# Kernel optimization log

Measured on AMD Instinct MI355X. Metric: run time of the kernel, lower is better.

## Reference

```python
import jax, jax.numpy as jnp
import numpy as np

D_MODEL = 256
NUM_HEADS = 4
EPS = 1e-6


def setup_inputs() -> dict:
    key = jax.random.key(0)
    ks = jax.random.split(key, 9)
    B, T, D = 4, 2048, D_MODEL
    scale = 1.0 / np.sqrt(D)
    inp = {
        "x": jax.random.normal(ks[0], (B, T, D), dtype=jnp.float32),
        "Wq": jax.random.normal(ks[1], (D, D), dtype=jnp.float32) * scale,
        "bq": jnp.zeros((D,), dtype=jnp.float32),
        "Wk": jax.random.normal(ks[2], (D, D), dtype=jnp.float32) * scale,
        "bk": jnp.zeros((D,), dtype=jnp.float32),
        "Wv": jax.random.normal(ks[3], (D, D), dtype=jnp.float32) * scale,
        "bv": jnp.zeros((D,), dtype=jnp.float32),
        "Wo": jax.random.normal(ks[4], (D, D), dtype=jnp.float32) * scale,
        "bo": jnp.zeros((D,), dtype=jnp.float32),
    }
    return inp


def _feature_map(a):
    # F.elu(x) + 1.0
    return jax.nn.elu(a) + 1.0


def reference(x, Wq, bq, Wk, bk, Wv, bv, Wo, bo):
    B, T, D = x.shape
    H = NUM_HEADS
    dh = D // H
    Q = _feature_map((x @ Wq + bq).reshape(B, T, H, dh))
    K = _feature_map((x @ Wk + bk).reshape(B, T, H, dh))
    V = (x @ Wv + bv).reshape(B, T, H, dh)
    # outer-product state: (B,T,H,dh,dh), cumulative over time
    KV = jnp.einsum('bthd,bthm->bthdm', K, V)
    S = jnp.cumsum(KV, axis=1)
    Z = jnp.cumsum(K, axis=1)
    out = jnp.einsum('bthd,bthdm->bthm', Q, S)
    denom = jnp.einsum('bthd,bthd->bth', Q, Z)[..., None] + EPS
    out = (out / denom).reshape(B, T, D)
    return out @ Wo + bo
```

## Files before the change

### kernel.cpp

```cpp
#include <hip/hip_runtime.h>
#include <hip/hip_bf16.h>

#define D_MODEL 256
#define NHEADS 4
#define DHEAD 64
#define BATCH 4
#define TSEQ 2048
#define CHUNK 64
#define NCHUNK (TSEQ / CHUNK)
#define NTOK (BATCH * TSEQ)
#define NBH (BATCH * NHEADS)
#define EPSV 1e-6f
#define LSTRF 68

typedef __bf16 bf16x8 __attribute__((ext_vector_type(8)));
typedef float f32x4 __attribute__((ext_vector_type(4)));
typedef unsigned short us8 __attribute__((ext_vector_type(8)));

__device__ __forceinline__ float elu1(float a) {
    return a > 0.0f ? a + 1.0f : __expf(a);
}

__device__ __forceinline__ unsigned short f2bf(float f) {
    __hip_bfloat16 h = __float2bfloat16(f);
    return __builtin_bit_cast(unsigned short, h);
}

__device__ __forceinline__ float bf2f(unsigned short u) {
    return __bfloat162float(__builtin_bit_cast(__hip_bfloat16, u));
}

__device__ __forceinline__ bf16x8 frag8(const float* p) {
    const float4 x = *reinterpret_cast<const float4*>(p);
    const float4 y = *reinterpret_cast<const float4*>(p + 4);
    us8 u;
    u[0] = f2bf(x.x); u[1] = f2bf(x.y); u[2] = f2bf(x.z); u[3] = f2bf(x.w);
    u[4] = f2bf(y.x); u[5] = f2bf(y.y); u[6] = f2bf(y.z); u[7] = f2bf(y.w);
    return __builtin_bit_cast(bf16x8, u);
}

__device__ __forceinline__ void gld_lds16(const void* g, void* l) {
    __builtin_amdgcn_global_load_lds(
        (const __attribute__((address_space(1))) void*)g,
        (__attribute__((address_space(3))) void*)l, 16, 0, 0);
}

__global__ __launch_bounds__(256) void convert_x_kernel(
    const float* __restrict__ x, unsigned short* __restrict__ xb)
{
    const int i = (blockIdx.x * 256 + threadIdx.x) * 8;
    const float4 a = *reinterpret_cast<const float4*>(&x[i]);
    const float4 b = *reinterpret_cast<const float4*>(&x[i + 4]);
    ushort4 u0 = { f2bf(a.x), f2bf(a.y), f2bf(a.z), f2bf(a.w) };
    ushort4 u1 = { f2bf(b.x), f2bf(b.y), f2bf(b.z), f2bf(b.w) };
    *reinterpret_cast<ushort4*>(&xb[i]) = u0;
    *reinterpret_cast<ushort4*>(&xb[i + 4]) = u1;
}

__global__ __launch_bounds__(256) void convert_w_kernel(
    const float* __restrict__ Wq, const float* __restrict__ Wk,
    const float* __restrict__ Wv, const float* __restrict__ Wo,
    unsigned short* __restrict__ Wt, unsigned short* __restrict__ Wot)
{
    __shared__ float Ls[64][65];
    const int tid = threadIdx.x;
    const int wi = blockIdx.x >> 4;
    const int ti = blockIdx.x & 15;
    const int k0 = (ti >> 2) * 64, n0 = (ti & 3) * 64;
    const float* W = wi == 0 ? Wq : wi == 1 ? Wk : wi == 2 ? Wv : Wo;
#pragma unroll
    for (int i = 0; i < 16; ++i) {
        const int idx = i * 256 + tid;
        const int r = idx >> 6, c = idx & 63;
        Ls[r][c] = W[(size_t)(k0 + r) * D_MODEL + n0 + c];
    }
    __syncthreads();
    unsigned short* outp = (wi < 3) ? (Wt + (size_t)(wi * 256 + n0) * D_MODEL + k0)
                                    : (Wot + (size_t)n0 * D_MODEL + k0);
#pragma unroll
    for (int i = 0; i < 16; ++i) {
        const int idx = i * 256 + tid;
        const int rn = idx >> 6, ck = idx & 63;
        outp[(size_t)rn * D_MODEL + ck] = f2bf(Ls[ck][rn]);
    }
}

template<int MODE>
__global__ __launch_bounds__(256) void mfma_gemm_kernel(
    const unsigned short* __restrict__ A,
    const unsigned short* __restrict__ Bt,
    const float* __restrict__ b0, const float* __restrict__ b1,
    const float* __restrict__ b2,
    void* __restrict__ O0, void* __restrict__ O1, void* __restrict__ O2)
{
    __shared__ __align__(16) unsigned short As[128 * 64];
    __shared__ __align__(16) unsigned short Bs[128 * 64];
    const int tid = threadIdx.x;
    const int wave = tid >> 6, lane = tid & 63;
    const int la = lane & 15, q = lane >> 4;
    const int wm = (wave >> 1) * 64, wn = (wave & 1) * 64;

    int mtile, ntile;
    if (MODE == 0) { ntile = blockIdx.x % 6; mtile = blockIdx.x / 6; }
    else           { ntile = blockIdx.x & 1; mtile = blockIdx.x >> 1; }
    const int m0 = mtile * 128, n0 = ntile * 128;

    const unsigned short* Ab = A  + (size_t)m0 * D_MODEL;
    const unsigned short* Bb = Bt + (size_t)n0 * D_MODEL;

    f32x4 acc[4][4];
#pragma unroll
    for (int i = 0; i < 4; ++i)
#pragma unroll
        for (int j = 0; j < 4; ++j) acc[i][j] = (f32x4){0.f, 0.f, 0.f, 0.f};

    for (int k0 = 0; k0 < D_MODEL; k0 += 64) {
#pragma unroll
        for (int i = 0; i < 4; ++i) {
            const int bslot = i * 256 + wave * 64;
            const int slot = bslot + lane;
            const int m = slot >> 3, s = slot & 7;
            const int g = s ^ (m & 7);
            gld_lds16(Ab + (size_t)m * D_MODEL + k0 + g * 8, &As[bslot * 8]);
            gld_lds16(Bb + (size_t)m * D_MODEL + k0 + g * 8, &Bs[bslot * 8]);
        }
        __syncthreads();

        bf16x8 af[4][2], bfr[4][2];
#pragma unroll
        for (int i = 0; i < 4; ++i) {
#pragma unroll
            for (int kh = 0; kh < 2; ++kh) {
                const int g = kh * 4 + q;
                const int m = wm + i * 16 + la;
                af[i][kh] = *reinterpret_cast<const bf16x8*>(
                    &As[m * 64 + ((g ^ (m & 7)) << 3)]);
                const int n = wn + i * 16 + la;
                bfr[i][kh] = *reinterpret_cast<const bf16x8*>(
                    &Bs[n * 64 + ((g ^ (n & 7)) << 3)]);
            }
        }
#pragma unroll
        for (int mi = 0; mi < 4; ++mi)
#pragma unroll
            for (int ni = 0; ni < 4; ++ni) {
                acc[mi][ni] = __builtin_amdgcn_mfma_f32_16x16x32_bf16(
                    af[mi][0], bfr[ni][0], acc[mi][ni], 0, 0, 0);
                acc[mi][ni] = __builtin_amdgcn_mfma_f32_16x16x32_bf16(
                    af[mi][1], bfr[ni][1], acc[mi][ni], 0, 0, 0);
            }
        __syncthreads();
    }

#pragma unroll
    for (int mi = 0; mi < 4; ++mi) {
#pragma unroll
        for (int ni = 0; ni < 4; ++ni) {
            const int row = m0 + wm + mi * 16 + q * 4;
            const int col = n0 + wn + ni * 16 + la;
            if (MODE == 0) {
                const int which = col >> 8;
                const int cl = col & 255;
                unsigned short* Out = (unsigned short*)
                    (which == 0 ? O0 : which == 1 ? O1 : O2);
                const float* bias = which == 0 ? b0 : which == 1 ? b1 : b2;
                const int act = (which < 2);
                const float bv = bias[cl];
#pragma unroll
                for (int r = 0; r < 4; ++r) {
                    float v = acc[mi][ni][r] + bv;
                    if (act) v = elu1(v);
                    Out[(size_t)(row + r) * D_MODEL + cl] = f2bf(v);
                }
            } else {
                float* Out = (float*)O0;
                const float bv = b0[col];
#pragma unroll
                for (int r = 0; r < 4; ++r)
                    Out[(size_t)(row + r) * D_MODEL + col] = acc[mi][ni][r] + bv;
            }
        }
    }
}

__global__ __launch_bounds__(256) void chunksum_kernel(
    const unsigned short* __restrict__ Kb, const unsigned short* __restrict__ Vb,
    float* __restrict__ Pt, float* __restrict__ Zc)
{
    __shared__ float Ktf[DHEAD * LSTRF];
    __shared__ float Vtf[DHEAD * LSTRF];
    const int tid = threadIdx.x;
    const int c  = blockIdx.x % NCHUNK;
    const int bh = blockIdx.x / NCHUNK;
    const int b = bh / NHEADS, h = bh % NHEADS;
    const size_t gbase = ((size_t)(b * TSEQ + c * CHUNK)) * D_MODEL + h * DHEAD;

#pragma unroll
    for (int i = 0; i < 16; ++i) {
        const int idx = i * 256 + tid;
        const int t = idx >> 6, d = idx & 63;
        Ktf[d * LSTRF + t] = bf2f(Kb[gbase + (size_t)t * D_MODEL + d]);
        Vtf[d * LSTRF + t] = bf2f(Vb[gbase + (size_t)t * D_MODEL + d]);
    }
    __syncthreads();

    const int wave = tid >> 6, lane = tid & 63;
    const int la = lane & 15, q = lane >> 4;
    const int wm = (wave >> 1) * 32, wn = (wave & 1) * 32;

    f32x4 acc[2][2];
#pragma unroll
    for (int i = 0; i < 2; ++i)
#pragma unroll
        for (int j = 0; j < 2; ++j) acc[i][j] = (f32x4){0.f, 0.f, 0.f, 0.f};

#pragma unroll
    for (int ks = 0; ks < 2; ++ks) {
        const int ko = ks * 32 + q * 8;
        const bf16x8 a0  = frag8(&Vtf[(wm + la) * LSTRF + ko]);
        const bf16x8 a1  = frag8(&Vtf[(wm + 16 + la) * LSTRF + ko]);
        const bf16x8 bb0 = frag8(&Ktf[(wn + la) * LSTRF + ko]);
        const bf16x8 bb1 = frag8(&Ktf[(wn + 16 + la) * LSTRF + ko]);
        acc[0][0] = __builtin_amdgcn_mfma_f32_16x16x32_bf16(a0, bb0, acc[0][0], 0, 0, 0);
        acc[0][1] = __builtin_amdgcn_mfma_f32_16x16x32_bf16(a0, bb1, acc[0][1], 0, 0, 0);
        acc[1][0] = __builtin_amdgcn_mfma_f32_16x16x32_bf16(a1, bb0, acc[1][0], 0, 0, 0);
        acc[1][1] = __builtin_amdgcn_mfma_f32_16x16x32_bf16(a1, bb1, acc[1][1], 0, 0, 0);
    }

    float* Pb = Pt + (size_t)blockIdx.x * (DHEAD * DHEAD);
#pragma unroll
    for (int mi = 0; mi < 2; ++mi)
#pragma unroll
        for (int ni = 0; ni < 2; ++ni) {
            const int row = wm + mi * 16 + q * 4;
            const int col = wn + ni * 16 + la;
#pragma unroll
            for (int r = 0; r < 4; ++r)
                Pb[(row + r) * DHEAD + col] = acc[mi][ni][r];
        }

    if (tid < DHEAD) {
        float z = 0.f;
        for (int t = 0; t < CHUNK; ++t) z += Ktf[tid * LSTRF + t];
        Zc[(size_t)blockIdx.x * DHEAD + tid] = z;
    }
}

__global__ __launch_bounds__(256) void prefix_kernel(
    float* __restrict__ P, float* __restrict__ Zc)
{
    const int tid = threadIdx.x;
    if (blockIdx.x < NBH * 16) {
        const int bh = blockIdx.x >> 4;
        const int e = ((blockIdx.x & 15) << 8) + tid;
        const size_t base = (size_t)bh * NCHUNK * (DHEAD * DHEAD) + e;
        float v[NCHUNK];
#pragma unroll
        for (int c = 0; c < NCHUNK; ++c) v[c] = P[base + (size_t)c * (DHEAD * DHEAD)];
        float s = 0.f;
#pragma unroll
        for (int c = 0; c < NCHUNK; ++c) {
            const float t = v[c];
            P[base + (size_t)c * (DHEAD * DHEAD)] = s;
            s += t;
        }
    } else {
        const int j = ((int)(blockIdx.x - NBH * 16) << 8) + tid;
        if (j < NBH * DHEAD) {
            const int bh = j >> 6, d = j & 63;
            float v[NCHUNK];
#pragma unroll
            for (int c = 0; c < NCHUNK; ++c) v[c] = Zc[(bh * NCHUNK + c) * DHEAD + d];
            float s = 0.f;
#pragma unroll
            for (int c = 0; c < NCHUNK; ++c) {
                const float t = v[c];
                Zc[(bh * NCHUNK + c) * DHEAD + d] = s;
                s += t;
            }
        }
    }
}

__global__ __launch_bounds__(256) void chunkout_kernel(
    const unsigned short* __restrict__ Qb, const unsigned short* __restrict__ Kb,
    const unsigned short* __restrict__ Vb,
    const float* __restrict__ Pt, const float* __restrict__ Zx,
    unsigned short* __restrict__ Ob)
{
    __shared__ float Qs[CHUNK * LSTRF];
    __shared__ float Ks[CHUNK * LSTRF];
    __shared__ float Vtf[DHEAD * LSTRF];
    __shared__ float At[CHUNK * LSTRF];
    __shared__ float zsh[DHEAD];
    __shared__ float dnm[CHUNK];

    const int tid = threadIdx.x;
    const int c  = blockIdx.x % NCHUNK;
    const int bh = blockIdx.x / NCHUNK;
    const int b = bh / NHEADS, h = bh % NHEADS;
    const size_t gbase = ((size_t)(b * TSEQ + c * CHUNK)) * D_MODEL + h * DHEAD;
    const float* Pp = Pt + (size_t)blockIdx.x * (DHEAD * DHEAD);

#pragma unroll
    for (int i = 0; i < 16; ++i) {
        const int idx = i * 256 + tid;
        const int t = idx >> 6, d = idx & 63;
        const float qv = bf2f(Qb[gbase + (size_t)t * D_MODEL + d]);
        const float kv = bf2f(Kb[gbase + (size_t)t * D_MODEL + d]);
        const float vv = bf2f(Vb[gbase + (size_t)t * D_MODEL + d]);
        Qs[t * LSTRF + d]  = qv;
        Ks[t * LSTRF + d]  = kv;
        Vtf[d * LSTRF + t] = vv;
    }
    if (tid < DHEAD) zsh[tid] = Zx[((size_t)bh * NCHUNK + c) * DHEAD + tid];
    __syncthreads();

    const int wave = tid >> 6, lane = tid & 63;
    const int la = lane & 15, q = lane >> 4;
    const int wt = (wave >> 1) * 32, wn = (wave & 1) * 32;

    f32x4 acc[2][2];
#pragma unroll
    for (int i = 0; i < 2; ++i)
#pragma unroll
        for (int j = 0; j < 2; ++j) acc[i][j] = (f32x4){0.f, 0.f, 0.f, 0.f};
#pragma unroll
    for (int ks = 0; ks < 2; ++ks) {
        const int ko = ks * 32 + q * 8;
        const bf16x8 a0  = frag8(&Qs[(wt + la) * LSTRF + ko]);
        const bf16x8 a1  = frag8(&Qs[(wt + 16 + la) * LSTRF + ko]);
        const bf16x8 bb0 = frag8(&Ks[(wn + la) * LSTRF + ko]);
        const bf16x8 bb1 = frag8(&Ks[(wn + 16 + la) * LSTRF + ko]);
        acc[0][0] = __builtin_amdgcn_mfma_f32_16x16x32_bf16(a0, bb0, acc[0][0], 0, 0, 0);
        acc[0][1] = __builtin_amdgcn_mfma_f32_16x16x32_bf16(a0, bb1, acc[0][1], 0, 0, 0);
        acc[1][0] = __builtin_amdgcn_mfma_f32_16x16x32_bf16(a1, bb0, acc[1][0], 0, 0, 0);
        acc[1][1] = __builtin_amdgcn_mfma_f32_16x16x32_bf16(a1, bb1, acc[1][1], 0, 0, 0);
    }
#pragma unroll
    for (int mi = 0; mi < 2; ++mi)
#pragma unroll
        for (int ni = 0; ni < 2; ++ni) {
            const int t0 = wt + mi * 16 + q * 4;
            const int s  = wn + ni * 16 + la;
#pragma unroll
            for (int r = 0; r < 4; ++r)
                At[(t0 + r) * LSTRF + s] = (s <= t0 + r) ? acc[mi][ni][r] : 0.f;
        }
    __syncthreads();

    if (tid < CHUNK) {
        float dv = 0.f;
        for (int s = 0; s < CHUNK; ++s) dv += At[tid * LSTRF + s];
        for (int d = 0; d < DHEAD; ++d) dv = fmaf(Qs[tid * LSTRF + d], zsh[d], dv);
        dnm[tid] = dv + EPSV;
    }
    __syncthreads();

    f32x4 o[2][2];
#pragma unroll
    for (int i = 0; i < 2; ++i)
#pragma unroll
        for (int j = 0; j < 2; ++j) o[i][j] = (f32x4){0.f, 0.f, 0.f, 0.f};
#pragma unroll
    for (int ks = 0; ks < 2; ++ks) {
        const int ko = ks * 32 + q * 8;
        const bf16x8 a0  = frag8(&Qs[(wt + la) * LSTRF + ko]);
        const bf16x8 a1  = frag8(&Qs[(wt + 16 + la) * LSTRF + ko]);
        const bf16x8 bb0 = frag8(&Pp[(wn + la) * DHEAD + ko]);
        const bf16x8 bb1 = frag8(&Pp[(wn + 16 + la) * DHEAD + ko]);
        o[0][0] = __builtin_amdgcn_mfma_f32_16x16x32_bf16(a0, bb0, o[0][0], 0, 0, 0);
        o[0][1] = __builtin_amdgcn_mfma_f32_16x16x32_bf16(a0, bb1, o[0][1], 0, 0, 0);
        o[1][0] = __builtin_amdgcn_mfma_f32_16x16x32_bf16(a1, bb0, o[1][0], 0, 0, 0);
        o[1][1] = __builtin_amdgcn_mfma_f32_16x16x32_bf16(a1, bb1, o[1][1], 0, 0, 0);
    }
#pragma unroll
    for (int ks = 0; ks < 2; ++ks) {
        const int ko = ks * 32 + q * 8;
        const bf16x8 a0  = frag8(&At[(wt + la) * LSTRF + ko]);
        const bf16x8 a1  = frag8(&At[(wt + 16 + la) * LSTRF + ko]);
        const bf16x8 bb0 = frag8(&Vtf[(wn + la) * LSTRF + ko]);
        const bf16x8 bb1 = frag8(&Vtf[(wn + 16 + la) * LSTRF + ko]);
        o[0][0] = __builtin_amdgcn_mfma_f32_16x16x32_bf16(a0, bb0, o[0][0], 0, 0, 0);
        o[0][1] = __builtin_amdgcn_mfma_f32_16x16x32_bf16(a0, bb1, o[0][1], 0, 0, 0);
        o[1][0] = __builtin_amdgcn_mfma_f32_16x16x32_bf16(a1, bb0, o[1][0], 0, 0, 0);
        o[1][1] = __builtin_amdgcn_mfma_f32_16x16x32_bf16(a1, bb1, o[1][1], 0, 0, 0);
    }

#pragma unroll
    for (int mi = 0; mi < 2; ++mi)
#pragma unroll
        for (int ni = 0; ni < 2; ++ni) {
            const int t0 = wt + mi * 16 + q * 4;
            const int m  = wn + ni * 16 + la;
#pragma unroll
            for (int r = 0; r < 4; ++r) {
                const float v = o[mi][ni][r] / dnm[t0 + r];
                Ob[gbase + (size_t)(t0 + r) * D_MODEL + m] = f2bf(v);
            }
        }
}

extern "C" void kernel_launch(void* const* d_in, const int* in_sizes, int n_in,
                              void* d_out, int out_size, void* d_ws, size_t ws_size,
                              hipStream_t stream)
{
    const float* x  = (const float*)d_in[0];
    const float* Wq = (const float*)d_in[1];
    const float* bq = (const float*)d_in[2];
    const float* Wk = (const float*)d_in[3];
    const float* bk = (const float*)d_in[4];
    const float* Wv = (const float*)d_in[5];
    const float* bv = (const float*)d_in[6];
    const float* Wo = (const float*)d_in[7];
    const float* bo = (const float*)d_in[8];
    float* out = (float*)d_out;

    const size_t NE = (size_t)NTOK * D_MODEL;
    unsigned short* xb  = (unsigned short*)d_ws;
    unsigned short* Wt  = xb + NE;
    unsigned short* Wot = Wt + 768 * 256;
    unsigned short* Qb  = Wot + 256 * 256;
    unsigned short* Kb  = Qb + NE;
    unsigned short* Vb  = Kb + NE;
    unsigned short* Ob  = Vb + NE;
    float* P = (float*)(Ob + NE);
    float* Z = P + (size_t)NBH * NCHUNK * DHEAD * DHEAD;

    convert_x_kernel<<<NTOK * D_MODEL / 8 / 256, 256, 0, stream>>>(x, xb);
    convert_w_kernel<<<64, 256, 0, stream>>>(Wq, Wk, Wv, Wo, Wt, Wot);
    mfma_gemm_kernel<0><<<(NTOK / 128) * 6, 256, 0, stream>>>(
        xb, Wt, bq, bk, bv, Qb, Kb, Vb);
    chunksum_kernel<<<NBH * NCHUNK, 256, 0, stream>>>(Kb, Vb, P, Z);
    prefix_kernel<<<NBH * 16 + 4, 256, 0, stream>>>(P, Z);
    chunkout_kernel<<<NBH * NCHUNK, 256, 0, stream>>>(Qb, Kb, Vb, P, Z, Ob);
    mfma_gemm_kernel<1><<<(NTOK / 128) * 2, 256, 0, stream>>>(
        Ob, Wot, bo, nullptr, nullptr, out, nullptr, nullptr);
}
```

Baseline: 117.0 us.

## Fuse chunked linear-attention stages into one sequential scan kernel per head slice

Replaces the chunksum, prefix-sum and chunkout kernels with a single scan kernel that walks all 32 chunks serially per (batch, head, 16-column slice). The running KV state and normalizer stay in shared memory, which removes the global P/Z buffers and two kernel launches. The x and W conversion kernels are also merged into one launch. The trade-off is a grid of only 64 blocks, each running a long serial loop with many barriers. Every block also recomputes Q·K^T for its chunk, so that work is repeated four times per head.

```diff
diff --git a/kernel.cpp b/kernel.cpp
--- a/kernel.cpp
+++ b/kernel.cpp
@@ -45,27 +45,28 @@
         (__attribute__((address_space(3))) void*)l, 16, 0, 0);
 }
 
-__global__ __launch_bounds__(256) void convert_x_kernel(
-    const float* __restrict__ x, unsigned short* __restrict__ xb)
-{
-    const int i = (blockIdx.x * 256 + threadIdx.x) * 8;
-    const float4 a = *reinterpret_cast<const float4*>(&x[i]);
-    const float4 b = *reinterpret_cast<const float4*>(&x[i + 4]);
-    ushort4 u0 = { f2bf(a.x), f2bf(a.y), f2bf(a.z), f2bf(a.w) };
-    ushort4 u1 = { f2bf(b.x), f2bf(b.y), f2bf(b.z), f2bf(b.w) };
-    *reinterpret_cast<ushort4*>(&xb[i]) = u0;
-    *reinterpret_cast<ushort4*>(&xb[i + 4]) = u1;
-}
-
-__global__ __launch_bounds__(256) void convert_w_kernel(
+__global__ __launch_bounds__(256) void convert_kernel(
+    const float* __restrict__ x,
     const float* __restrict__ Wq, const float* __restrict__ Wk,
     const float* __restrict__ Wv, const float* __restrict__ Wo,
+    unsigned short* __restrict__ xb,
     unsigned short* __restrict__ Wt, unsigned short* __restrict__ Wot)
 {
+    const int tid = threadIdx.x;
+    if (blockIdx.x < NTOK * D_MODEL / 8 / 256) {
+        const int i = (blockIdx.x * 256 + tid) * 8;
+        const float4 a = *reinterpret_cast<const float4*>(&x[i]);
+        const float4 b = *reinterpret_cast<const float4*>(&x[i + 4]);
+        ushort4 u0 = { f2bf(a.x), f2bf(a.y), f2bf(a.z), f2bf(a.w) };
+        ushort4 u1 = { f2bf(b.x), f2bf(b.y), f2bf(b.z), f2bf(b.w) };
+        *reinterpret_cast<ushort4*>(&xb[i]) = u0;
+        *reinterpret_cast<ushort4*>(&xb[i + 4]) = u1;
+        return;
+    }
     __shared__ float Ls[64][65];
-    const int tid = threadIdx.x;
-    const int wi = blockIdx.x >> 4;
-    const int ti = blockIdx.x & 15;
+    const int bid = blockIdx.x - NTOK * D_MODEL / 8 / 256;
+    const int wi = bid >> 4;
+    const int ti = bid & 15;
     const int k0 = (ti >> 2) * 64, n0 = (ti & 3) * 64;
     const float* W = wi == 0 ? Wq : wi == 1 ? Wk : wi == 2 ? Wv : Wo;
 #pragma unroll
@@ -183,222 +184,148 @@
     }
 }
 
-__global__ __launch_bounds__(256) void chunksum_kernel(
-    const unsigned short* __restrict__ Kb, const unsigned short* __restrict__ Vb,
-    float* __restrict__ Pt, float* __restrict__ Zc)
+__global__ __launch_bounds__(256) void scan_kernel(
+    const unsigned short* __restrict__ Qb, const unsigned short* __restrict__ Kb,
+    const unsigned short* __restrict__ Vb, unsigned short* __restrict__ Ob)
 {
-    __shared__ float Ktf[DHEAD * LSTRF];
-    __shared__ float Vtf[DHEAD * LSTRF];
+    __shared__ float Qs[64 * LSTRF];
+    __shared__ float Ks[64 * LSTRF];
+    __shared__ float AtKt[64 * LSTRF];
+    __shared__ float Vt[16 * LSTRF];
+    __shared__ float St[16 * LSTRF];
+    __shared__ float zsh[64];
+    __shared__ float part[64 * 5];
+    __shared__ float zp[64 * 5];
+
     const int tid = threadIdx.x;
-    const int c  = blockIdx.x % NCHUNK;
-    const int bh = blockIdx.x / NCHUNK;
-    const int b = bh / NHEADS, h = bh % NHEADS;
-    const size_t gbase = ((size_t)(b * TSEQ + c * CHUNK)) * D_MODEL + h * DHEAD;
-
-#pragma unroll
-    for (int i = 0; i < 16; ++i) {
-        const int idx = i * 256 + tid;
-        const int t = idx >> 6, d = idx & 63;
-        Ktf[d * LSTRF + t] = bf2f(Kb[gbase + (size_t)t * D_MODEL + d]);
-        Vtf[d * LSTRF + t] = bf2f(Vb[gbase + (size_t)t * D_MODEL + d]);
-    }
-    __syncthreads();
-
     const int wave = tid >> 6, lane = tid & 63;
     const int la = lane & 15, q = lane >> 4;
-    const int wm = (wave >> 1) * 32, wn = (wave & 1) * 32;
-
-    f32x4 acc[2][2];
-#pragma unroll
-    for (int i = 0; i < 2; ++i)
-#pragma unroll
-        for (int j = 0; j < 2; ++j) acc[i][j] = (f32x4){0.f, 0.f, 0.f, 0.f};
-
-#pragma unroll
-    for (int ks = 0; ks < 2; ++ks) {
-        const int ko = ks * 32 + q * 8;
-        const bf16x8 a0  = frag8(&Vtf[(wm + la) * LSTRF + ko]);
-        const bf16x8 a1  = frag8(&Vtf[(wm + 16 + la) * LSTRF + ko]);
-        const bf16x8 bb0 = frag8(&Ktf[(wn + la) * LSTRF + ko]);
-        const bf16x8 bb1 = frag8(&Ktf[(wn + 16 + la) * LSTRF + ko]);
-        acc[0][0] = __builtin_amdgcn_mfma_f32_16x16x32_bf16(a0, bb0, acc[0][0], 0, 0, 0);
-        acc[0][1] = __builtin_amdgcn_mfma_f32_16x16x32_bf16(a0, bb1, acc[0][1], 0, 0, 0);
-        acc[1][0] = __builtin_amdgcn_mfma_f32_16x16x32_bf16(a1, bb0, acc[1][0], 0, 0, 0);
-        acc[1][1] = __builtin_amdgcn_mfma_f32_16x16x32_bf16(a1, bb1, acc[1][1], 0, 0, 0);
-    }
-
-    float* Pb = Pt + (size_t)blockIdx.x * (DHEAD * DHEAD);
-#pragma unroll
-    for (int mi = 0; mi < 2; ++mi)
-#pragma unroll
-        for (int ni = 0; ni < 2; ++ni) {
-            const int row = wm + mi * 16 + q * 4;
-            const int col = wn + ni * 16 + la;
+    const int td = tid & 63, q4 = tid >> 6;
+    const int bh = blockIdx.x >> 2, mh = blockIdx.x & 3;
+    const int b = bh >> 2, h = bh & 3;
+    const size_t hbase = (size_t)b * TSEQ * D_MODEL + h * DHEAD;
+
+    for (int i = tid; i < 16 * LSTRF; i += 256) St[i] = 0.f;
+    if (tid < 64) zsh[tid] = 0.f;
+    __syncthreads();
+
+    for (int c = 0; c < NCHUNK; ++c) {
+        const size_t gq = hbase + (size_t)c * CHUNK * D_MODEL;
+
+#pragma unroll
+        for (int i = 0; i < 16; ++i) {
+            const int idx = i * 256 + tid;
+            const int t = idx >> 6, d = idx & 63;
+            Qs[t * LSTRF + d] = bf2f(Qb[gq + (size_t)t * D_MODEL + d]);
+            Ks[t * LSTRF + d] = bf2f(Kb[gq + (size_t)t * D_MODEL + d]);
+        }
+#pragma unroll
+        for (int i = 0; i < 4; ++i) {
+            const int idx = i * 256 + tid;
+            const int t = idx >> 4, m = idx & 15;
+            Vt[m * LSTRF + t] = bf2f(Vb[gq + (size_t)t * D_MODEL + mh * 16 + m]);
+        }
+        __syncthreads();
+
+        {
+            const int wt2 = (wave >> 1) * 32, wn2 = (wave & 1) * 32;
+            f32x4 acc[2][2];
+#pragma unroll
+            for (int i = 0; i < 2; ++i)
+#pragma unroll
+                for (int j = 0; j < 2; ++j) acc[i][j] = (f32x4){0.f, 0.f, 0.f, 0.f};
+#pragma unroll
+            for (int ks = 0; ks < 2; ++ks) {
+                const int ko = ks * 32 + q * 8;
+                const bf16x8 a0  = frag8(&Qs[(wt2 + la) * LSTRF + ko]);
+                const bf16x8 a1  = frag8(&Qs[(wt2 + 16 + la) * LSTRF + ko]);
+                const bf16x8 bb0 = frag8(&Ks[(wn2 + la) * LSTRF + ko]);
+                const bf16x8 bb1 = frag8(&Ks[(wn2 + 16 + la) * LSTRF + ko]);
+                acc[0][0] = __builtin_amdgcn_mfma_f32_16x16x32_bf16(a0, bb0, acc[0][0], 0, 0, 0);
+                acc[0][1] = __builtin_amdgcn_mfma_f32_16x16x32_bf16(a0, bb1, acc[0][1], 0, 0, 0);
+                acc[1][0] = __builtin_amdgcn_mfma_f32_16x16x32_bf16(a1, bb0, acc[1][0], 0, 0, 0);
+                acc[1][1] = __builtin_amdgcn_mfma_f32_16x16x32_bf16(a1, bb1, acc[1][1], 0, 0, 0);
+            }
+#pragma unroll
+            for (int mi = 0; mi < 2; ++mi)
+#pragma unroll
+                for (int ni = 0; ni < 2; ++ni) {
+                    const int t0 = wt2 + mi * 16 + q * 4;
+                    const int s  = wn2 + ni * 16 + la;
+#pragma unroll
+                    for (int r = 0; r < 4; ++r)
+                        AtKt[(t0 + r) * LSTRF + s] =
+                            (s <= t0 + r) ? acc[mi][ni][r] : 0.f;
+                }
+        }
+        {
+            float zv = 0.f;
+            for (int t = q4 * 16; t < q4 * 16 + 16; ++t) zv += Ks[t * LSTRF + td];
+            zp[td * 5 + q4] = zv;
+        }
+        __syncthreads();
+
+        {
+            float pv = 0.f;
+            for (int s = q4 * 16; s < q4 * 16 + 16; ++s) pv += AtKt[td * LSTRF + s];
+            for (int d = q4 * 16; d < q4 * 16 + 16; ++d)
+                pv = fmaf(Qs[td * LSTRF + d], zsh[d], pv);
+            part[td * 5 + q4] = pv;
+        }
+        __syncthreads();
+
+        {
+            f32x4 o = (f32x4){0.f, 0.f, 0.f, 0.f};
+#pragma unroll
+            for (int ks = 0; ks < 2; ++ks) {
+                const int ko = ks * 32 + q * 8;
+                const bf16x8 aQ = frag8(&Qs[(wave * 16 + la) * LSTRF + ko]);
+                const bf16x8 bS = frag8(&St[la * LSTRF + ko]);
+                o = __builtin_amdgcn_mfma_f32_16x16x32_bf16(aQ, bS, o, 0, 0, 0);
+            }
+#pragma unroll
+            for (int ks = 0; ks < 2; ++ks) {
+                const int ko = ks * 32 + q * 8;
+                const bf16x8 aA = frag8(&AtKt[(wave * 16 + la) * LSTRF + ko]);
+                const bf16x8 bV = frag8(&Vt[la * LSTRF + ko]);
+                o = __builtin_amdgcn_mfma_f32_16x16x32_bf16(aA, bV, o, 0, 0, 0);
+            }
+#pragma unroll
+            for (int r = 0; r < 4; ++r) {
+                const int t = wave * 16 + q * 4 + r;
+                const float dn = part[t * 5 + 0] + part[t * 5 + 1]
+                               + part[t * 5 + 2] + part[t * 5 + 3] + EPSV;
+                Ob[gq + (size_t)t * D_MODEL + mh * 16 + la] = f2bf(o[r] / dn);
+            }
+        }
+        __syncthreads();
+
+#pragma unroll
+        for (int i = 0; i < 16; ++i) {
+            const int idx = i * 256 + tid;
+            const int t = idx >> 6, d = idx & 63;
+            AtKt[d * LSTRF + t] = Ks[t * LSTRF + d];
+        }
+        __syncthreads();
+
+        {
+            f32x4 su = (f32x4){0.f, 0.f, 0.f, 0.f};
+#pragma unroll
+            for (int ks = 0; ks < 2; ++ks) {
+                const int ko = ks * 32 + q * 8;
+                const bf16x8 aV = frag8(&Vt[la * LSTRF + ko]);
+                const bf16x8 bK = frag8(&AtKt[(wave * 16 + la) * LSTRF + ko]);
+                su = __builtin_amdgcn_mfma_f32_16x16x32_bf16(aV, bK, su, 0, 0, 0);
+            }
 #pragma unroll
             for (int r = 0; r < 4; ++r)
-                Pb[(row + r) * DHEAD + col] = acc[mi][ni][r];
-        }
-
-    if (tid < DHEAD) {
-        float z = 0.f;
-        for (int t = 0; t < CHUNK; ++t) z += Ktf[tid * LSTRF + t];
-        Zc[(size_t)blockIdx.x * DHEAD + tid] = z;
-    }
-}
-
-__global__ __launch_bounds__(256) void prefix_kernel(
-    float* __restrict__ P, float* __restrict__ Zc)
-{
-    const int tid = threadIdx.x;
-    if (blockIdx.x < NBH * 16) {
-        const int bh = blockIdx.x >> 4;
-        const int e = ((blockIdx.x & 15) << 8) + tid;
-        const size_t base = (size_t)bh * NCHUNK * (DHEAD * DHEAD) + e;
-        float v[NCHUNK];
-#pragma unroll
-        for (int c = 0; c < NCHUNK; ++c) v[c] = P[base + (size_t)c * (DHEAD * DHEAD)];
-        float s = 0.f;
-#pragma unroll
-        for (int c = 0; c < NCHUNK; ++c) {
-            const float t = v[c];
-            P[base + (size_t)c * (DHEAD * DHEAD)] = s;
-            s += t;
-        }
-    } else {
-        const int j = ((int)(blockIdx.x - NBH * 16) << 8) + tid;
-        if (j < NBH * DHEAD) {
-            const int bh = j >> 6, d = j & 63;
-            float v[NCHUNK];
-#pragma unroll
-            for (int c = 0; c < NCHUNK; ++c) v[c] = Zc[(bh * NCHUNK + c) * DHEAD + d];
-            float s = 0.f;
-#pragma unroll
-            for (int c = 0; c < NCHUNK; ++c) {
-                const float t = v[c];
-                Zc[(bh * NCHUNK + c) * DHEAD + d] = s;
-                s += t;
-            }
-        }
-    }
-}
-
-__global__ __launch_bounds__(256) void chunkout_kernel(
-    const unsigned short* __restrict__ Qb, const unsigned short* __restrict__ Kb,
-    const unsigned short* __restrict__ Vb,
-    const float* __restrict__ Pt, const float* __restrict__ Zx,
-    unsigned short* __restrict__ Ob)
-{
-    __shared__ float Qs[CHUNK * LSTRF];
-    __shared__ float Ks[CHUNK * LSTRF];
-    __shared__ float Vtf[DHEAD * LSTRF];
-    __shared__ float At[CHUNK * LSTRF];
-    __shared__ float zsh[DHEAD];
-    __shared__ float dnm[CHUNK];
-
-    const int tid = threadIdx.x;
-    const int c  = blockIdx.x % NCHUNK;
-    const int bh = blockIdx.x / NCHUNK;
-    const int b = bh / NHEADS, h = bh % NHEADS;
-    const size_t gbase = ((size_t)(b * TSEQ + c * CHUNK)) * D_MODEL + h * DHEAD;
-    const float* Pp = Pt + (size_t)blockIdx.x * (DHEAD * DHEAD);
-
-#pragma unroll
-    for (int i = 0; i < 16; ++i) {
-        const int idx = i * 256 + tid;
-        const int t = idx >> 6, d = idx & 63;
-        const float qv = bf2f(Qb[gbase + (size_t)t * D_MODEL + d]);
-        const float kv = bf2f(Kb[gbase + (size_t)t * D_MODEL + d]);
-        const float vv = bf2f(Vb[gbase + (size_t)t * D_MODEL + d]);
-        Qs[t * LSTRF + d]  = qv;
-        Ks[t * LSTRF + d]  = kv;
-        Vtf[d * LSTRF + t] = vv;
-    }
-    if (tid < DHEAD) zsh[tid] = Zx[((size_t)bh * NCHUNK + c) * DHEAD + tid];
-    __syncthreads();
-
-    const int wave = tid >> 6, lane = tid & 63;
-    const int la = lane & 15, q = lane >> 4;
-    const int wt = (wave >> 1) * 32, wn = (wave & 1) * 32;
-
-    f32x4 acc[2][2];
-#pragma unroll
-    for (int i = 0; i < 2; ++i)
-#pragma unroll
-        for (int j = 0; j < 2; ++j) acc[i][j] = (f32x4){0.f, 0.f, 0.f, 0.f};
-#pragma unroll
-    for (int ks = 0; ks < 2; ++ks) {
-        const int ko = ks * 32 + q * 8;
-        const bf16x8 a0  = frag8(&Qs[(wt + la) * LSTRF + ko]);
-        const bf16x8 a1  = frag8(&Qs[(wt + 16 + la) * LSTRF + ko]);
-        const bf16x8 bb0 = frag8(&Ks[(wn + la) * LSTRF + ko]);
-        const bf16x8 bb1 = frag8(&Ks[(wn + 16 + la) * LSTRF + ko]);
-        acc[0][0] = __builtin_amdgcn_mfma_f32_16x16x32_bf16(a0, bb0, acc[0][0], 0, 0, 0);
-        acc[0][1] = __builtin_amdgcn_mfma_f32_16x16x32_bf16(a0, bb1, acc[0][1], 0, 0, 0);
-        acc[1][0] = __builtin_amdgcn_mfma_f32_16x16x32_bf16(a1, bb0, acc[1][0], 0, 0, 0);
-        acc[1][1] = __builtin_amdgcn_mfma_f32_16x16x32_bf16(a1, bb1, acc[1][1], 0, 0, 0);
-    }
-#pragma unroll
-    for (int mi = 0; mi < 2; ++mi)
-#pragma unroll
-        for (int ni = 0; ni < 2; ++ni) {
-            const int t0 = wt + mi * 16 + q * 4;
-            const int s  = wn + ni * 16 + la;
-#pragma unroll
-            for (int r = 0; r < 4; ++r)
-                At[(t0 + r) * LSTRF + s] = (s <= t0 + r) ? acc[mi][ni][r] : 0.f;
-        }
-    __syncthreads();
-
-    if (tid < CHUNK) {
-        float dv = 0.f;
-        for (int s = 0; s < CHUNK; ++s) dv += At[tid * LSTRF + s];
-        for (int d = 0; d < DHEAD; ++d) dv = fmaf(Qs[tid * LSTRF + d], zsh[d], dv);
-        dnm[tid] = dv + EPSV;
-    }
-    __syncthreads();
-
-    f32x4 o[2][2];
-#pragma unroll
-    for (int i = 0; i < 2; ++i)
-#pragma unroll
-        for (int j = 0; j < 2; ++j) o[i][j] = (f32x4){0.f, 0.f, 0.f, 0.f};
-#pragma unroll
-    for (int ks = 0; ks < 2; ++ks) {
-        const int ko = ks * 32 + q * 8;
-        const bf16x8 a0  = frag8(&Qs[(wt + la) * LSTRF + ko]);
-        const bf16x8 a1  = frag8(&Qs[(wt + 16 + la) * LSTRF + ko]);
-        const bf16x8 bb0 = frag8(&Pp[(wn + la) * DHEAD + ko]);
-        const bf16x8 bb1 = frag8(&Pp[(wn + 16 + la) * DHEAD + ko]);
-        o[0][0] = __builtin_amdgcn_mfma_f32_16x16x32_bf16(a0, bb0, o[0][0], 0, 0, 0);
-        o[0][1] = __builtin_amdgcn_mfma_f32_16x16x32_bf16(a0, bb1, o[0][1], 0, 0, 0);
-        o[1][0] = __builtin_amdgcn_mfma_f32_16x16x32_bf16(a1, bb0, o[1][0], 0, 0, 0);
-        o[1][1] = __builtin_amdgcn_mfma_f32_16x16x32_bf16(a1, bb1, o[1][1], 0, 0, 0);
-    }
-#pragma unroll
-    for (int ks = 0; ks < 2; ++ks) {
-        const int ko = ks * 32 + q * 8;
-        const bf16x8 a0  = frag8(&At[(wt + la) * LSTRF + ko]);
-        const bf16x8 a1  = frag8(&At[(wt + 16 + la) * LSTRF + ko]);
-        const bf16x8 bb0 = frag8(&Vtf[(wn + la) * LSTRF + ko]);
-        const bf16x8 bb1 = frag8(&Vtf[(wn + 16 + la) * LSTRF + ko]);
-        o[0][0] = __builtin_amdgcn_mfma_f32_16x16x32_bf16(a0, bb0, o[0][0], 0, 0, 0);
-        o[0][1] = __builtin_amdgcn_mfma_f32_16x16x32_bf16(a0, bb1, o[0][1], 0, 0, 0);
-        o[1][0] = __builtin_amdgcn_mfma_f32_16x16x32_bf16(a1, bb0, o[1][0], 0, 0, 0);
-        o[1][1] = __builtin_amdgcn_mfma_f32_16x16x32_bf16(a1, bb1, o[1][1], 0, 0, 0);
-    }
-
-#pragma unroll
-    for (int mi = 0; mi < 2; ++mi)
-#pragma unroll
-        for (int ni = 0; ni < 2; ++ni) {
-            const int t0 = wt + mi * 16 + q * 4;
-            const int m  = wn + ni * 16 + la;
-#pragma unroll
-            for (int r = 0; r < 4; ++r) {
-                const float v = o[mi][ni][r] / dnm[t0 + r];
-                Ob[gbase + (size_t)(t0 + r) * D_MODEL + m] = f2bf(v);
-            }
-        }
+                St[(q * 4 + r) * LSTRF + wave * 16 + la] += su[r];
+        }
+        if (tid < 64)
+            zsh[tid] += zp[tid * 5 + 0] + zp[tid * 5 + 1]
+                      + zp[tid * 5 + 2] + zp[tid * 5 + 3];
+        __syncthreads();
+    }
 }
 
 extern "C" void kernel_launch(void* const* d_in, const int* in_sizes, int n_in,
@@ -424,16 +351,12 @@
     unsigned short* Kb  = Qb + NE;
     unsigned short* Vb  = Kb + NE;
     unsigned short* Ob  = Vb + NE;
-    float* P = (float*)(Ob + NE);
-    float* Z = P + (size_t)NBH * NCHUNK * DHEAD * DHEAD;
-
-    convert_x_kernel<<<NTOK * D_MODEL / 8 / 256, 256, 0, stream>>>(x, xb);
-    convert_w_kernel<<<64, 256, 0, stream>>>(Wq, Wk, Wv, Wo, Wt, Wot);
+
+    convert_kernel<<<NTOK * D_MODEL / 8 / 256 + 64, 256, 0, stream>>>(
+        x, Wq, Wk, Wv, Wo, xb, Wt, Wot);
     mfma_gemm_kernel<0><<<(NTOK / 128) * 6, 256, 0, stream>>>(
         xb, Wt, bq, bk, bv, Qb, Kb, Vb);
-    chunksum_kernel<<<NBH * NCHUNK, 256, 0, stream>>>(Kb, Vb, P, Z);
-    prefix_kernel<<<NBH * 16 + 4, 256, 0, stream>>>(P, Z);
-    chunkout_kernel<<<NBH * NCHUNK, 256, 0, stream>>>(Qb, Kb, Vb, P, Z, Ob);
+    scan_kernel<<<NBH * 4, 256, 0, stream>>>(Qb, Kb, Vb, Ob);
     mfma_gemm_kernel<1><<<(NTOK / 128) * 2, 256, 0, stream>>>(
         Ob, Wot, bo, nullptr, nullptr, out, nullptr, nullptr);
 }
```

After: 219.7 us. +87.8%, slower.
